# Optimization experiments

Measured on AMD Instinct MI355X. Metric: run time of the kernel, lower is better.

Reference implementation:

```python
import jax, jax.numpy as jnp
import numpy as np

B, N, D_IN, D_OUT = 8, 2048, 512, 512


def setup_inputs() -> dict:
    key = jax.random.key(0)
    ks = jax.random.split(key, 9)
    s = 1.0 / np.sqrt(D_IN)
    return {
        "x": jax.random.normal(ks[0], (B, N, D_IN), dtype=jnp.float32),
        "adj": jax.random.uniform(ks[1], (B, N, N), dtype=jnp.float32, maxval=3.0),
        "Wq": jax.random.uniform(ks[2], (D_IN, D_OUT), jnp.float32, -s, s),
        "bq": jax.random.uniform(ks[3], (D_OUT,), jnp.float32, -s, s),
        "Wk": jax.random.uniform(ks[4], (D_IN, D_OUT), jnp.float32, -s, s),
        "bk": jax.random.uniform(ks[5], (D_OUT,), jnp.float32, -s, s),
        "Wv": jax.random.uniform(ks[6], (D_IN, D_OUT), jnp.float32, -s, s),
        "bv": jax.random.uniform(ks[7], (D_OUT,), jnp.float32, -s, s),
        "scale": jnp.float32(1.0),
        "width": jnp.float32(2.0),
    }


def reference(x, adj, Wq, bq, Wk, bk, Wv, bv, scale, width):
    # Linear projections
    Q = jnp.einsum("bnd,de->bne", x, Wq) + bq
    K = jnp.einsum("bnd,de->bne", x, Wk) + bk
    V = jnp.einsum("bnd,de->bne", x, Wv) + bv
    inv_sqrt_d = 1.0 / jnp.sqrt(jnp.float32(D_OUT))
    scores = jnp.einsum("bqe,bke->bqk", Q, K) * inv_sqrt_d  # [B,N,N]
    # Learned Gaussian distance mask, multiplicatively fused into scores
    masks = jnp.exp(-((adj - scale) ** 2 / width))
    attn = jax.nn.softmax(scores * masks, axis=-1)
    return jnp.einsum("bqk,bke->bqe", attn, V)
```

## Files before the change

### kernel.cpp

```cpp
#include <hip/hip_runtime.h>
#include <hip/hip_bf16.h>
#include <cstdint>

typedef __attribute__((ext_vector_type(4))) float f32x4;
typedef __attribute__((ext_vector_type(8))) short s16x8;

#define LOG2E 1.44269504088896340736f

#define WAITV0 asm volatile("s_waitcnt vmcnt(0)" ::: "memory")
#define WAITV2 asm volatile("s_waitcnt vmcnt(2)" ::: "memory")
#define WAITLG asm volatile("s_waitcnt lgkmcnt(0)" ::: "memory")

__device__ __forceinline__ unsigned short f2bf(float f) {
    unsigned int u = __builtin_bit_cast(unsigned int, f);
    u += 0x7FFFu + ((u >> 16) & 1u);
    return (unsigned short)(u >> 16);
}
__device__ __forceinline__ float bf2f(unsigned short u) {
    return __builtin_bit_cast(float, (unsigned int)u << 16);
}
__device__ __forceinline__ void gload_lds16(const void* g, void* l) {
    __builtin_amdgcn_global_load_lds(
        (const __attribute__((address_space(1))) unsigned int*)g,
        (__attribute__((address_space(3))) unsigned int*)l, 16, 0, 0);
}
__device__ __forceinline__ int m3(int v) {
    if (v >= 9) v -= 9;
    if (v >= 6) v -= 6;
    if (v >= 3) v -= 3;
    return v;
}


__global__ void convert_x_kernel(const float* __restrict__ x,
                                 unsigned short* __restrict__ xb, int n4) {
    int i = blockIdx.x * blockDim.x + threadIdx.x;
    if (i < n4) {
        const float4 v = reinterpret_cast<const float4*>(x)[i];
        ushort4 o;
        o.x = f2bf(v.x); o.y = f2bf(v.y); o.z = f2bf(v.z); o.w = f2bf(v.w);
        reinterpret_cast<ushort4*>(xb)[i] = o;
    }
}

__global__ void transpose_w_kernel(const float* __restrict__ Wq,
                                   const float* __restrict__ Wk,
                                   const float* __restrict__ Wv,
                                   unsigned short* __restrict__ WT) {
    int i = blockIdx.x * blockDim.x + threadIdx.x;
    int m = i >> 18;
    int r = i & 262143;
    int n = r & 511;
    int k = r >> 9;
    const float* W = (m == 0) ? Wq : (m == 1) ? Wk : Wv;
    WT[(m << 18) + n * 512 + k] = f2bf(W[k * 512 + n]);
}

__global__ __launch_bounds__(256, 2) void proj_gemm_kernel(
    const unsigned short* __restrict__ xb,
    const unsigned short* __restrict__ WT,
    const float* __restrict__ bq, const float* __restrict__ bk, const float* __restrict__ bv,
    unsigned short* __restrict__ Qb, unsigned short* __restrict__ Kb,
    unsigned short* __restrict__ VT)
{
    const int z = blockIdx.z;
    const unsigned short* Wt = WT + (z << 18);
    const float* bias = (z == 0) ? bq : (z == 1) ? bk : bv;

    const int gm = blockIdx.x * 128;
    const int gn = blockIdx.y * 128;
    const int wave = threadIdx.x >> 6, lane = threadIdx.x & 63;
    const int wr = wave >> 1, wc = wave & 1;
    const int lr = lane & 15, lg = lane >> 4;
    const int row0 = gm + wr * 64;
    const int col0 = gn + wc * 64;

    f32x4 acc[4][4];
    #pragma unroll
    for (int mi = 0; mi < 4; mi++)
        #pragma unroll
        for (int ni = 0; ni < 4; ni++)
            acc[mi][ni] = (f32x4){0.f, 0.f, 0.f, 0.f};

    for (int k0 = 0; k0 < 512; k0 += 32) {
        s16x8 a[4], b[4];
        #pragma unroll
        for (int mi = 0; mi < 4; mi++)
            a[mi] = *reinterpret_cast<const s16x8*>(xb + (size_t)(row0 + mi * 16 + lr) * 512 + k0 + lg * 8);
        #pragma unroll
        for (int ni = 0; ni < 4; ni++)
            b[ni] = *reinterpret_cast<const s16x8*>(Wt + (size_t)(col0 + ni * 16 + lr) * 512 + k0 + lg * 8);
        #pragma unroll
        for (int mi = 0; mi < 4; mi++)
            #pragma unroll
            for (int ni = 0; ni < 4; ni++)
                acc[mi][ni] = __builtin_amdgcn_mfma_f32_16x16x32_bf16(a[mi], b[ni], acc[mi][ni], 0, 0, 0);
    }

    #pragma unroll
    for (int ni = 0; ni < 4; ni++) {
        const int col = col0 + ni * 16 + lr;
        const float bs = bias[col];
        #pragma unroll
        for (int mi = 0; mi < 4; mi++) {
            const int rowb = row0 + mi * 16 + lg * 4;
            if (z == 2) {
                unsigned short h[4];
                #pragma unroll
                for (int j = 0; j < 4; j++) h[j] = f2bf(acc[mi][ni][j] + bs);
                const int bb = rowb >> 11;
                const int nn = rowb & 2047;
                ushort4 o; o.x = h[0]; o.y = h[1]; o.z = h[2]; o.w = h[3];
                *reinterpret_cast<ushort4*>(VT + (size_t)bb * (512 * 2048) + (size_t)col * 2048 + nn) = o;
            } else {
                unsigned short* dst = (z == 0) ? Qb : Kb;
                #pragma unroll
                for (int j = 0; j < 4; j++)
                    dst[(size_t)(rowb + j) * 512 + col] = f2bf(acc[mi][ni][j] + bs);
            }
        }
    }
}

__global__ __launch_bounds__(512, 2) void attn_kernel(
    const unsigned short* __restrict__ Qb,
    const unsigned short* __restrict__ Kb,
    const unsigned short* __restrict__ VTb,
    const float* __restrict__ adj,
    const float* __restrict__ scale_p, const float* __restrict__ width_p,
    unsigned short* __restrict__ Op,
    float* __restrict__ Mp, float* __restrict__ Lp)
{
    const int bk   = blockIdx.x;
    const int b    = bk >> 1;
    const int kvh  = bk & 1;
    const int qt   = blockIdx.y;
    const int wave = threadIdx.x >> 6;
    const int lane = threadIdx.x & 63;
    const int lr   = lane & 15;
    const int lg   = lane >> 4;

    __shared__ __align__(16) char smem[68096];
    char* kring = smem;
    char* vring = smem + 24576;
    unsigned short (*pbuf)[4][16][72] = (unsigned short (*)[4][16][72])(smem + 49152);
    float* corrbuf = (float*)(smem + 67584);

    if (wave < 4) {
        const int sw = wave;
        const int q0 = qt * 64 + sw * 16;
        const unsigned short* Qrow = Qb + ((size_t)b * 2048 + q0) * 512;
        const char* Kg = (const char*)Kb + ((size_t)b * 2048 + (size_t)kvh * 1024) * 1024;
        const float* adj_b = adj + (size_t)b * 2048 * 2048
                           + (size_t)(q0 + lg * 4) * 2048 + (size_t)kvh * 1024 + lr;
        const float scl = *scale_p;
        const float nw  = -LOG2E / (*width_p);
        const float cf  = 0.044194173824159216f * LOG2E;

        auto stage_k = [&](int slot, int c) {
            char* dstb = kring + slot * 8192;
            const int kvt = (c >> 3) * 64;
            const int dcb = (c & 7) * 128;
            #pragma unroll
            for (int i = 0; i < 2; i++) {
                const int sl  = sw * 2 + i;
                const int row = sl * 8 + (lane >> 3);
                const int colb = (lane & 7) * 16;
                gload_lds16(Kg + (size_t)(kvt + row) * 1024 + dcb + (colb ^ ((row & 7) << 4)),
                            dstb + sl * 1024);
            }
        };

        s16x8 qf[16];
        #pragma unroll
        for (int ks = 0; ks < 16; ks++)
            qf[ks] = __builtin_nontemporal_load(
                reinterpret_cast<const s16x8*>(Qrow + (size_t)lr * 512 + ks * 32 + lg * 8));

        f32x4 sacc[4];
        #pragma unroll
        for (int nt = 0; nt < 4; nt++) sacc[nt] = (f32x4){0.f, 0.f, 0.f, 0.f};
        float m_[4] = {-1e30f, -1e30f, -1e30f, -1e30f};
        float l_[4] = {0.f, 0.f, 0.f, 0.f};

        stage_k(0, 0);
        stage_k(1, 1);
        WAITV0;
        __builtin_amdgcn_s_barrier();

        int rcur = 0;
        for (int t = 0; t < 16; ++t) {
            const int kv0 = t * 64;
            float av[4][4];
            #pragma unroll
            for (int p = 0; p < 8; ++p) {
                if (p == 6) {
                    #pragma unroll
                    for (int nt = 0; nt < 4; nt++)
                        #pragma unroll
                        for (int j = 0; j < 4; j++)
                            av[nt][j] = __builtin_nontemporal_load(
                                &adj_b[(size_t)j * 2048 + kv0 + nt * 16]);
                }
                const bool do_stage = (t < 15) || (p < 6);
                if (do_stage) stage_k(m3(rcur + p + 2), t * 8 + p + 2);

                const char* kb_ = kring + m3(rcur + p) * 8192;
                __builtin_amdgcn_s_setprio(1);
                #pragma unroll
                for (int ks = 0; ks < 2; ks++) {
                    const s16x8 a = qf[p * 2 + ks];
                    #pragma unroll
                    for (int nt = 0; nt < 4; nt++) {
                        const int row = nt * 16 + lr;
                        const int cbyte = ks * 64 + lg * 16;
                        const s16x8 kf = *reinterpret_cast<const s16x8*>(
                            kb_ + row * 128 + (cbyte ^ ((row & 7) << 4)));
                        sacc[nt] = __builtin_amdgcn_mfma_f32_16x16x32_bf16(a, kf, sacc[nt], 0, 0, 0);
                    }
                }
                __builtin_amdgcn_s_setprio(0);

                if (p == 7) {
                    #pragma unroll
                    for (int nt = 0; nt < 4; nt++)
                        #pragma unroll
                        for (int j = 0; j < 4; j++) {
                            const float d = av[nt][j] - scl;
                            sacc[nt][j] = sacc[nt][j] * cf * exp2f(d * d * nw);
                        }
                    float corr[4];
                    #pragma unroll
                    for (int j = 0; j < 4; j++) {
                        float v = fmaxf(fmaxf(sacc[0][j], sacc[1][j]), fmaxf(sacc[2][j], sacc[3][j]));
                        #pragma unroll
                        for (int sh = 1; sh < 16; sh <<= 1) v = fmaxf(v, __shfl_xor(v, sh, 64));
                        const float mn = fmaxf(m_[j], v);
                        corr[j] = exp2f(m_[j] - mn);
                        m_[j] = mn;
                    }
                    #pragma unroll
                    for (int j = 0; j < 4; j++) {
                        float rs = 0.f;
                        #pragma unroll
                        for (int nt = 0; nt < 4; nt++) {
                            const float pv = exp2f(sacc[nt][j] - m_[j]);
                            pbuf[t & 1][sw][lg * 4 + j][nt * 16 + lr] = f2bf(pv);
                            rs += pv;
                        }
                        #pragma unroll
                        for (int sh = 1; sh < 16; sh <<= 1) rs += __shfl_xor(rs, sh, 64);
                        l_[j] = l_[j] * corr[j] + rs;
                    }
                    if (lr == 0) {
                        #pragma unroll
                        for (int j = 0; j < 4; j++)
                            corrbuf[(t & 1) * 64 + sw * 16 + lg * 4 + j] = corr[j];
                    }
                    #pragma unroll
                    for (int nt = 0; nt < 4; nt++) sacc[nt] = (f32x4){0.f, 0.f, 0.f, 0.f};
                    WAITLG;
                }
                if (do_stage) { WAITV2; } else { WAITV0; }
                __builtin_amdgcn_s_barrier();
            }
            rcur += 2; if (rcur >= 3) rcur -= 3;
        }
        #pragma unroll
        for (int p = 0; p < 8; ++p) {
            WAITV0;
            __builtin_amdgcn_s_barrier();
        }
        const size_t prow0 = (size_t)kvh * 16384 + (size_t)b * 2048 + q0;
        if (lr == 0) {
            #pragma unroll
            for (int j = 0; j < 4; j++) {
                Mp[prow0 + lg * 4 + j] = m_[j];
                Lp[prow0 + lg * 4 + j] = l_[j];
            }
        }
    } else {
        const int ow = wave - 4;
        const int q0 = qt * 64 + ow * 16;
        const char* Vg = (const char*)VTb + ((size_t)b * 512 * 2048 + (size_t)kvh * 1024) * 2;

        auto stage_v = [&](int slot, int c) {
            char* dstb = vring + slot * 8192;
            const int kvt = (c >> 3) * 64;
            const int dr0 = (c & 7) * 64;
            #pragma unroll
            for (int i = 0; i < 2; i++) {
                const int sl  = ow * 2 + i;
                const int row = sl * 8 + (lane >> 3);
                const int colb = (lane & 7) * 16;
                gload_lds16(Vg + (size_t)(dr0 + row) * 4096 + (size_t)kvt * 2 + (colb ^ ((row & 7) << 4)),
                            dstb + sl * 1024);
            }
        };

        f32x4 oacc[32];
        #pragma unroll
        for (int i = 0; i < 32; i++) oacc[i] = (f32x4){0.f, 0.f, 0.f, 0.f};
        s16x8 pa0{}, pa1{};

        __builtin_amdgcn_s_barrier();

        #pragma unroll
        for (int p = 0; p < 8; ++p) {
            if (p == 6) stage_v(0, 0);
            if (p == 7) stage_v(1, 1);
            WAITV2;
            __builtin_amdgcn_s_barrier();
        }

        int rcur = 2;
        for (int t = 1; t < 17; ++t) {
            #pragma unroll
            for (int p = 0; p < 8; ++p) {
                const bool do_stage = (t < 16) || (p < 6);
                if (do_stage) stage_v(m3(rcur + p), t * 8 + p - 6);

                if (p == 0) {
                    const float* cl = corrbuf + ((t - 1) & 1) * 64 + ow * 16;
                    float c_[4];
                    #pragma unroll
                    for (int j = 0; j < 4; j++) c_[j] = cl[lg * 4 + j];
                    const unsigned short* pb = &pbuf[(t - 1) & 1][ow][0][0];
                    pa0 = *reinterpret_cast<const s16x8*>(pb + lr * 72 + lg * 8);
                    pa1 = *reinterpret_cast<const s16x8*>(pb + lr * 72 + 32 + lg * 8);
                    const bool need = __any(c_[0] < 1.f || c_[1] < 1.f || c_[2] < 1.f || c_[3] < 1.f);
                    if (need) {
                        #pragma unroll
                        for (int f = 0; f < 32; f++)
                            #pragma unroll
                            for (int j = 0; j < 4; j++) oacc[f][j] *= c_[j];
                    }
                }

                const char* vb_ = vring + m3(rcur + p + 1) * 8192;
                __builtin_amdgcn_s_setprio(1);
                #pragma unroll
                for (int ks2 = 0; ks2 < 2; ks2++) {
                    const s16x8 pa = (ks2 == 0) ? pa0 : pa1;
                    #pragma unroll
                    for (int df2 = 0; df2 < 4; df2++) {
                        const int row = df2 * 16 + lr;
                        const int cbyte = ks2 * 64 + lg * 16;
                        const s16x8 vf = *reinterpret_cast<const s16x8*>(
                            vb_ + row * 128 + (cbyte ^ ((row & 7) << 4)));
                        oacc[p * 4 + df2] = __builtin_amdgcn_mfma_f32_16x16x32_bf16(pa, vf, oacc[p * 4 + df2], 0, 0, 0);
                    }
                }
                __builtin_amdgcn_s_setprio(0);

                if (do_stage) { WAITV2; } else { WAITV0; }
                __builtin_amdgcn_s_barrier();
            }
            rcur += 2; if (rcur >= 3) rcur -= 3;
        }

        unsigned short* lds_t = (unsigned short*)smem + (size_t)ow * 4224;
        const size_t prow0 = (size_t)kvh * 16384 + (size_t)b * 2048 + q0;
        #pragma unroll
        for (int h = 0; h < 2; ++h) {
            #pragma unroll
            for (int dd = 0; dd < 16; ++dd) {
                const int df = h * 16 + dd;
                #pragma unroll
                for (int j = 0; j < 4; ++j)
                    lds_t[(lg * 4 + j) * 264 + dd * 16 + lr] = f2bf(oacc[df][j]);
            }
            #pragma unroll
            for (int g2 = 0; g2 < 2; ++g2) {
                const int r16  = g2 * 8 + (lane >> 3);
                const int colu = (lane & 7) * 8;
                unsigned short* oprow = Op + (prow0 + r16) * 512 + h * 256;
                #pragma unroll
                for (int k = 0; k < 4; ++k) {
                    const s16x8 v = *reinterpret_cast<const s16x8*>(&lds_t[r16 * 264 + colu + k * 64]);
                    __builtin_nontemporal_store(v, reinterpret_cast<s16x8*>(oprow + colu + k * 64));
                }
            }
        }
    }
}

__global__ void combine_kernel(const unsigned short* __restrict__ Op,
                               const float* __restrict__ Mp, const float* __restrict__ Lp,
                               float* __restrict__ out) {
    const int idx = blockIdx.x * 256 + threadIdx.x;
    const int r   = idx >> 6;
    const int c8  = (idx & 63) * 8;
    const float m0 = Mp[r], m1 = Mp[16384 + r];
    const float l0 = Lp[r], l1 = Lp[16384 + r];
    const float M  = fmaxf(m0, m1);
    const float e0 = exp2f(m0 - M), e1 = exp2f(m1 - M);
    const float invL = 1.f / (e0 * l0 + e1 * l1);
    const s16x8 a = __builtin_nontemporal_load(
        reinterpret_cast<const s16x8*>(Op + (size_t)r * 512 + c8));
    const s16x8 bq = __builtin_nontemporal_load(
        reinterpret_cast<const s16x8*>(Op + (size_t)16384 * 512 + (size_t)r * 512 + c8));
    float o[8];
    #pragma unroll
    for (int i = 0; i < 8; i++)
        o[i] = (bf2f((unsigned short)a[i]) * e0 + bf2f((unsigned short)bq[i]) * e1) * invL;
    f32x4* dst = reinterpret_cast<f32x4*>(out + (size_t)r * 512 + c8);
    __builtin_nontemporal_store((f32x4){o[0], o[1], o[2], o[3]}, dst);
    __builtin_nontemporal_store((f32x4){o[4], o[5], o[6], o[7]}, dst + 1);
}


extern "C" void kernel_launch(void* const* d_in, const int* in_sizes, int n_in,
                              void* d_out, int out_size, void* d_ws, size_t ws_size,
                              hipStream_t stream) {
    const float* x     = (const float*)d_in[0];
    const float* adj   = (const float*)d_in[1];
    const float* Wq    = (const float*)d_in[2];
    const float* bq    = (const float*)d_in[3];
    const float* Wk    = (const float*)d_in[4];
    const float* bk    = (const float*)d_in[5];
    const float* Wv    = (const float*)d_in[6];
    const float* bv    = (const float*)d_in[7];
    const float* scale = (const float*)d_in[8];
    const float* width = (const float*)d_in[9];

    char* ws = (char*)d_ws;
    unsigned short* xb = (unsigned short*)(ws);
    unsigned short* WT = (unsigned short*)(ws + 16777216);
    unsigned short* Qb = (unsigned short*)(ws + 18350080);
    unsigned short* Kb = (unsigned short*)(ws + 35127296);
    unsigned short* VT = (unsigned short*)(ws + 51904512);
    unsigned short* Op = (unsigned short*)(ws + 68681728);
    float*          Mp = (float*)(ws + 102236160);
    float*          Lp = (float*)(ws + 102367232);
    float* out = (float*)d_out;

    hipLaunchKernelGGL(convert_x_kernel, dim3(8192), dim3(256), 0, stream, x, xb, 8388608 / 4);
    hipLaunchKernelGGL(transpose_w_kernel, dim3(3072), dim3(256), 0, stream, Wq, Wk, Wv, WT);
    hipLaunchKernelGGL(proj_gemm_kernel, dim3(128, 4, 3), dim3(256), 0, stream,
                       xb, WT, bq, bk, bv, Qb, Kb, VT);
    hipLaunchKernelGGL(attn_kernel, dim3(16, 32), dim3(512), 0, stream,
                       Qb, Kb, VT, adj, scale, width, Op, Mp, Lp);
    hipLaunchKernelGGL(combine_kernel, dim3(4096), dim3(256), 0, stream, Op, Mp, Lp, out);
}
```

Measured before the change: 290.1 us.

## Stage projection GEMM through double-buffered LDS and coalesce transposes and epilogue stores

The projection GEMM now loads A and B tiles with global_load_lds into double-buffered shared memory, 64-wide in K, instead of each wave reading fragments directly from global memory. The epilogue goes through a padded LDS tile so Q, K and the transposed V are written as coalesced 16-byte nontemporal stores rather than scattered 2-byte or 8-byte writes. The weight transpose kernel also uses a shared-memory tile so both its reads and writes are coalesced. In exchange the GEMM uses 36 KB of LDS per block and a barrier per K step, which may limit occupancy.

```diff
diff --git a/kernel.cpp b/kernel.cpp
--- a/kernel.cpp
+++ b/kernel.cpp
@@ -10,6 +10,7 @@
 #define WAITV0 asm volatile("s_waitcnt vmcnt(0)" ::: "memory")
 #define WAITV2 asm volatile("s_waitcnt vmcnt(2)" ::: "memory")
 #define WAITLG asm volatile("s_waitcnt lgkmcnt(0)" ::: "memory")
+#define BARRIER asm volatile("s_barrier" ::: "memory")
 
 __device__ __forceinline__ unsigned short f2bf(float f) {
     unsigned int u = __builtin_bit_cast(unsigned int, f);
@@ -47,25 +48,35 @@
                                    const float* __restrict__ Wk,
                                    const float* __restrict__ Wv,
                                    unsigned short* __restrict__ WT) {
-    int i = blockIdx.x * blockDim.x + threadIdx.x;
-    int m = i >> 18;
-    int r = i & 262143;
-    int n = r & 511;
-    int k = r >> 9;
-    const float* W = (m == 0) ? Wq : (m == 1) ? Wk : Wv;
-    WT[(m << 18) + n * 512 + k] = f2bf(W[k * 512 + n]);
+    const int z = blockIdx.z;
+    const int n0 = blockIdx.x * 64, k0 = blockIdx.y * 64;
+    const float* W = (z == 0) ? Wq : (z == 1) ? Wk : Wv;
+    __shared__ float tile[64][65];
+    const int tx = threadIdx.x & 63, ty = threadIdx.x >> 6;
+    #pragma unroll
+    for (int i = 0; i < 16; ++i) {
+        const int r = i * 4 + ty;
+        tile[r][tx] = W[(size_t)(k0 + r) * 512 + n0 + tx];
+    }
+    __syncthreads();
+    #pragma unroll
+    for (int i = 0; i < 16; ++i) {
+        const int r = i * 4 + ty;
+        WT[(size_t)(z << 18) + (size_t)(n0 + r) * 512 + k0 + tx] = f2bf(tile[tx][r]);
+    }
 }
 
 __global__ __launch_bounds__(256, 2) void proj_gemm_kernel(
     const unsigned short* __restrict__ xb,
     const unsigned short* __restrict__ WT,
-    const float* __restrict__ bq, const float* __restrict__ bk, const float* __restrict__ bv,
+    const float* __restrict__ bq, const float* __restrict__ bkp, const float* __restrict__ bv,
     unsigned short* __restrict__ Qb, unsigned short* __restrict__ Kb,
     unsigned short* __restrict__ VT)
 {
     const int z = blockIdx.z;
-    const unsigned short* Wt = WT + (z << 18);
-    const float* bias = (z == 0) ? bq : (z == 1) ? bk : bv;
+    const char* Wt = (const char*)(WT + (z << 18));
+    const char* Xg = (const char*)xb;
+    const float* bias = (z == 0) ? bq : (z == 1) ? bkp : bv;
 
     const int gm = blockIdx.x * 128;
     const int gn = blockIdx.y * 128;
@@ -75,6 +86,21 @@
     const int row0 = gm + wr * 64;
     const int col0 = gn + wc * 64;
 
+    __shared__ __align__(16) char smem[36864];
+    char* As = smem;
+    char* Bs = smem + 16384;
+
+    auto stage = [&](int buf, int k0b) {
+        #pragma unroll
+        for (int i = 0; i < 2; ++i) {
+            const int s = wave * 2 + i;
+            const int row = s * 16 + (lane >> 2);
+            const int colb = (lane & 3) * 16;
+            gload_lds16(Xg + (size_t)(gm + row) * 1024 + k0b + colb, As + buf * 8192 + s * 1024);
+            gload_lds16(Wt + (size_t)(gn + row) * 1024 + k0b + colb, Bs + buf * 8192 + s * 1024);
+        }
+    };
+
     f32x4 acc[4][4];
     #pragma unroll
     for (int mi = 0; mi < 4; mi++)
@@ -82,42 +108,71 @@
         for (int ni = 0; ni < 4; ni++)
             acc[mi][ni] = (f32x4){0.f, 0.f, 0.f, 0.f};
 
-    for (int k0 = 0; k0 < 512; k0 += 32) {
-        s16x8 a[4], b[4];
+    stage(0, 0);
+    WAITV0;
+    BARRIER;
+
+    int buf = 0;
+    for (int t = 0; t < 16; ++t) {
+        if (t < 15) stage(buf ^ 1, (t + 1) * 64);
+        s16x8 a[4], bfr[4];
         #pragma unroll
         for (int mi = 0; mi < 4; mi++)
-            a[mi] = *reinterpret_cast<const s16x8*>(xb + (size_t)(row0 + mi * 16 + lr) * 512 + k0 + lg * 8);
+            a[mi] = *reinterpret_cast<const s16x8*>(As + buf * 8192 + (wr * 64 + mi * 16 + lr) * 64 + lg * 16);
         #pragma unroll
         for (int ni = 0; ni < 4; ni++)
-            b[ni] = *reinterpret_cast<const s16x8*>(Wt + (size_t)(col0 + ni * 16 + lr) * 512 + k0 + lg * 8);
+            bfr[ni] = *reinterpret_cast<const s16x8*>(Bs + buf * 8192 + (wc * 64 + ni * 16 + lr) * 64 + lg * 16);
         #pragma unroll
         for (int mi = 0; mi < 4; mi++)
             #pragma unroll
             for (int ni = 0; ni < 4; ni++)
-                acc[mi][ni] = __builtin_amdgcn_mfma_f32_16x16x32_bf16(a[mi], b[ni], acc[mi][ni], 0, 0, 0);
+                acc[mi][ni] = __builtin_amdgcn_mfma_f32_16x16x32_bf16(a[mi], bfr[ni], acc[mi][ni], 0, 0, 0);
+        WAITV0;
+        BARRIER;
+        buf ^= 1;
     }
 
-    #pragma unroll
-    for (int ni = 0; ni < 4; ni++) {
-        const int col = col0 + ni * 16 + lr;
-        const float bs = bias[col];
-        #pragma unroll
-        for (int mi = 0; mi < 4; mi++) {
-            const int rowb = row0 + mi * 16 + lg * 4;
-            if (z == 2) {
-                unsigned short h[4];
-                #pragma unroll
-                for (int j = 0; j < 4; j++) h[j] = f2bf(acc[mi][ni][j] + bs);
-                const int bb = rowb >> 11;
-                const int nn = rowb & 2047;
-                ushort4 o; o.x = h[0]; o.y = h[1]; o.z = h[2]; o.w = h[3];
-                *reinterpret_cast<ushort4*>(VT + (size_t)bb * (512 * 2048) + (size_t)col * 2048 + nn) = o;
-            } else {
-                unsigned short* dst = (z == 0) ? Qb : Kb;
+    unsigned short* lt = (unsigned short*)smem + (size_t)wave * 4608;
+    if (z < 2) {
+        #pragma unroll
+        for (int ni = 0; ni < 4; ni++) {
+            const float bs = bias[col0 + ni * 16 + lr];
+            #pragma unroll
+            for (int mi = 0; mi < 4; mi++)
                 #pragma unroll
                 for (int j = 0; j < 4; j++)
-                    dst[(size_t)(rowb + j) * 512 + col] = f2bf(acc[mi][ni][j] + bs);
-            }
+                    lt[(mi * 16 + lg * 4 + j) * 72 + ni * 16 + lr] = f2bf(acc[mi][ni][j] + bs);
+        }
+        WAITLG;
+        unsigned short* dst = (z == 0) ? Qb : Kb;
+        #pragma unroll
+        for (int g2 = 0; g2 < 8; ++g2) {
+            const int r = g2 * 8 + (lane >> 3);
+            const int colu = (lane & 7) * 8;
+            const s16x8 v = *reinterpret_cast<const s16x8*>(&lt[r * 72 + colu]);
+            __builtin_nontemporal_store(v,
+                reinterpret_cast<s16x8*>(dst + (size_t)(row0 + r) * 512 + col0 + colu));
+        }
+    } else {
+        #pragma unroll
+        for (int ni = 0; ni < 4; ni++) {
+            const float bs = bias[col0 + ni * 16 + lr];
+            #pragma unroll
+            for (int mi = 0; mi < 4; mi++)
+                #pragma unroll
+                for (int j = 0; j < 4; j++)
+                    lt[(ni * 16 + lr) * 72 + mi * 16 + lg * 4 + j] = f2bf(acc[mi][ni][j] + bs);
+        }
+        WAITLG;
+        const int bb = row0 >> 11;
+        const int nn0 = row0 & 2047;
+        #pragma unroll
+        for (int g2 = 0; g2 < 8; ++g2) {
+            const int c = g2 * 8 + (lane >> 3);
+            const int colu = (lane & 7) * 8;
+            const s16x8 v = *reinterpret_cast<const s16x8*>(&lt[c * 72 + colu]);
+            __builtin_nontemporal_store(v,
+                reinterpret_cast<s16x8*>(VT + (size_t)bb * (512 * 2048) + (size_t)(col0 + c) * 2048 + nn0 + colu));
         }
     }
 }
@@ -436,7 +491,7 @@
     float* out = (float*)d_out;
 
     hipLaunchKernelGGL(convert_x_kernel, dim3(8192), dim3(256), 0, stream, x, xb, 8388608 / 4);
-    hipLaunchKernelGGL(transpose_w_kernel, dim3(3072), dim3(256), 0, stream, Wq, Wk, Wv, WT);
+    hipLaunchKernelGGL(transpose_w_kernel, dim3(8, 8, 3), dim3(256), 0, stream, Wq, Wk, Wv, WT);
     hipLaunchKernelGGL(proj_gemm_kernel, dim3(128, 4, 3), dim3(256), 0, stream,
                        xb, WT, bq, bk, bv, Qb, Kb, VT);
     hipLaunchKernelGGL(attn_kernel, dim3(16, 32), dim3(512), 0, stream,
```

Measured after the change: 240.7 us. -17.0%, faster.
